# Kernel optimization log

Measured on AMD Instinct MI355X. Metric: run time of the kernel, lower is better.

## Reference

```python
import jax, jax.numpy as jnp
import numpy as np

B, N, E, T, DIN, H, G, ND, NT, L = 4, 10000, 320000, 16, 16, 64, 64, 16, 3, 7


def _mlp2(x, W1, b1, W2, b2):
    # Linear -> LeakyReLU -> (Dropout: eval identity) -> Linear -> LeakyReLU
    h = jax.nn.leaky_relu(x @ W1 + b1)
    return jax.nn.leaky_relu(h @ W2 + b2)


def _gcn_conv(x, src, dst, ew, nt, W1, b1, W2, b2):
    # x: [B,N,D], nt: [B,N,ND], ew: [*,E,1] broadcastable over batch
    x_in = _mlp2(jnp.concatenate([x, nt], axis=-1), W1, b1, W2, b2)  # [B,N,G]
    msgs = x_in[:, src, :] * ew                                      # gather + weight, [B,E,G]
    aggr = jnp.zeros(x_in.shape, x_in.dtype).at[:, dst, :].add(msgs) # scatter-add, [B,N,G]
    return x + aggr


def _gru(x, Wx, Wh, bx, bh):
    # PyTorch-style GRU over time axis. x: [B,N,T,DIN] -> hs: [T,B,N,H]
    xw = jnp.einsum('bntd,dh->tbnh', x, Wx) + bx  # precompute input projections [T,B,N,3H]
    h0 = jnp.zeros(x.shape[:2] + (Wh.shape[0],), x.dtype)

    def step(h, xw_t):
        hw = h @ Wh + bh
        xr, xz, xn = jnp.split(xw_t, 3, axis=-1)
        hr, hz, hn = jnp.split(hw, 3, axis=-1)
        r = jax.nn.sigmoid(xr + hr)
        z = jax.nn.sigmoid(xz + hz)
        n = jnp.tanh(xn + r * hn)
        h_new = (1 - z) * n + z * h
        return h_new, h_new

    _, hs = jax.lax.scan(step, h0, xw)
    return hs


def reference(input_day, edge_attr, gru_Wx, gru_Wh, gru_bx, gru_bh,
              rnn_fc_W, rnn_fc_b,
              e_emb, e_c0_W1, e_c0_b1, e_c0_W2, e_c0_b2,
              e_c1_W1, e_c1_b1, e_c1_W2, e_c1_b2,
              e_fm_W1, e_fm_b1, e_fm_W2, e_fm_b2,
              g_emb, g_c0_W1, g_c0_b1, g_c0_W2, g_c0_b2,
              g_c1_W1, g_c1_b1, g_c1_W2, g_c1_b2,
              gcn_fc_W, gcn_fc_b,
              edge_index, node_type_ids):
    src, dst = edge_index[0], edge_index[1]

    # KRNN encoder (GRU) + max over time + FC head
    hs = _gru(input_day, gru_Wx, gru_Wh, gru_bx, gru_bh)  # [T,B,N,H]
    rnn_out = hs.max(axis=0)                              # kr_out.max(dim=-2) -> [B,N,H]
    y_rnn = rnn_out @ rnn_fc_W + rnn_fc_b                 # [B,N,L]

    # EdgeNet: GCN stack on static edge_attr, then per-edge pair MLP -> gate
    nt_e = jnp.broadcast_to(e_emb[node_type_ids][None], (B, N, ND))
    ew0 = edge_attr.reshape(1, E, 1)
    x = rnn_out
    x = _gcn_conv(x, src, dst, ew0, nt_e, e_c0_W1, e_c0_b1, e_c0_W2, e_c0_b2)
    x = _gcn_conv(x, src, dst, ew0, nt_e, e_c1_W1, e_c1_b1, e_c1_W2, e_c1_b2)
    edge_x = jnp.concatenate([x[:, src, :], x[:, dst, :]], axis=-1)  # [B,E,2G]
    h = jax.nn.leaky_relu(edge_x @ e_fm_W1 + e_fm_b1)
    edge_gate = jax.nn.relu(h @ e_fm_W2 + e_fm_b2)                   # [B,E,1]

    # Main GCNNet with learned edge gates
    nt_g = jnp.broadcast_to(g_emb[node_type_ids][None], (B, N, ND))
    x = rnn_out
    x = _gcn_conv(x, src, dst, edge_gate, nt_g, g_c0_W1, g_c0_b1, g_c0_W2, g_c0_b2)
    x = _gcn_conv(x, src, dst, edge_gate, nt_g, g_c1_W1, g_c1_b1, g_c1_W2, g_c1_b2)
    y_gcn = x @ gcn_fc_W + gcn_fc_b                                  # [B,N,L]

    return y_rnn + y_gcn


def setup_inputs() -> dict:
    key = jax.random.key(0)
    ks = iter(jax.random.split(key, 48))

    def nrm(shape, s=0.1):
        return jax.random.normal(next(ks), shape, jnp.float32) * s

    inp = {}
    inp['input_day'] = jax.random.normal(next(ks), (B, N, T, DIN), jnp.float32)
    inp['edge_index'] = jax.random.randint(next(ks), (2, E), 0, N)
    inp['node_type_ids'] = jax.random.randint(next(ks), (N,), 0, NT)
    inp['edge_attr'] = jax.random.uniform(next(ks), (E,), jnp.float32)

    inp['gru_Wx'] = nrm((DIN, 3 * H))
    inp['gru_Wh'] = nrm((H, 3 * H))
    inp['gru_bx'] = jnp.zeros((3 * H,), jnp.float32)
    inp['gru_bh'] = jnp.zeros((3 * H,), jnp.float32)
    inp['rnn_fc_W'] = nrm((H, L))
    inp['rnn_fc_b'] = jnp.zeros((L,), jnp.float32)

    inp['e_emb'] = nrm((NT, ND))
    inp['g_emb'] = nrm((NT, ND))
    for pre, in_dim in (('e_c0', H + ND), ('e_c1', G + ND), ('g_c0', H + ND), ('g_c1', G + ND)):
        inp[pre + '_W1'] = nrm((in_dim, G))
        inp[pre + '_b1'] = jnp.zeros((G,), jnp.float32)
        inp[pre + '_W2'] = nrm((G, G))
        inp[pre + '_b2'] = jnp.zeros((G,), jnp.float32)

    inp['e_fm_W1'] = nrm((2 * G, G))
    inp['e_fm_b1'] = jnp.zeros((G,), jnp.float32)
    inp['e_fm_W2'] = nrm((G, 1))
    inp['e_fm_b2'] = jnp.zeros((1,), jnp.float32)

    inp['gcn_fc_W'] = nrm((G, L))
    inp['gcn_fc_b'] = jnp.zeros((L,), jnp.float32)
    return inp
```

## Files before the change

kernel.cpp:

```cpp
#include <hip/hip_runtime.h>
#include <hip/hip_bf16.h>

#define NB 4
#define NN 10000
#define NE 320000
#define BN 40000
#define NL 7

typedef float f32x4 __attribute__((ext_vector_type(4)));
typedef __bf16 bf16x8 __attribute__((ext_vector_type(8)));

__device__ __forceinline__ float bf2f(unsigned short u){
  unsigned x = ((unsigned)u) << 16;
  return __builtin_bit_cast(float, x);
}
__device__ __forceinline__ unsigned short f2bf(float f){
  unsigned u = __builtin_bit_cast(unsigned, f);
  u += 0x7fffu + ((u >> 16) & 1u);
  return (unsigned short)(u >> 16);
}
__device__ __forceinline__ bf16x8 zero8(){
  uint4 z = make_uint4(0u,0u,0u,0u);
  return __builtin_bit_cast(bf16x8, z);
}
__device__ __forceinline__ bf16x8 one8(){
  uint4 z = make_uint4(0x3f80u,0u,0u,0u);
  return __builtin_bit_cast(bf16x8, z);
}
__device__ __forceinline__ bf16x8 ld8bf(const unsigned short* p){
  uint4 u = *(const uint4*)p;
  return __builtin_bit_cast(bf16x8, u);
}
__device__ __forceinline__ unsigned pk2(float lo, float hi){
  unsigned r;
  asm("v_cvt_pk_bf16_f32 %0, %1, %2" : "=v"(r) : "v"(lo), "v"(hi));
  return r;
}
__device__ __forceinline__ bf16x8 ld8f(const float* p){
  float4 a = *(const float4*)p;
  float4 b = *(const float4*)(p+4);
  uint4 u = make_uint4(pk2(a.x,a.y), pk2(a.z,a.w), pk2(b.x,b.y), pk2(b.z,b.w));
  return __builtin_bit_cast(bf16x8, u);
}
__device__ __forceinline__ float frcp(float x){ return __builtin_amdgcn_rcpf(x); }
__device__ __forceinline__ float tanh_(float x){ return 1.f - 2.f*frcp(__expf(2.f*x)+1.f); }
__device__ __forceinline__ float lrelu(float x){ return x > 0.f ? x : 0.01f*x; }

#define LDS_WAIT() asm volatile("s_waitcnt lgkmcnt(0)" ::: "memory")

#define WT_SET   10240
#define WT_UV    40960
#define WT_TOTAL 49152

__device__ __forceinline__ void mlp2_body(
    int bid,
    const float* __restrict__ x,
    const int* __restrict__ ntid,
    const float* __restrict__ emb,
    const unsigned short* __restrict__ W1T,
    const float* __restrict__ b1,
    const unsigned short* __restrict__ W2T,
    const float* __restrict__ b2,
    unsigned short* __restrict__ out)
{
  __shared__ __attribute__((aligned(16))) unsigned short hb[4][16][72];
  int tid = threadIdx.x;
  int wave = tid>>6, lane = tid&63, ln16 = lane&15, quad = lane>>4;
  int row0 = bid*64 + wave*16;
  int r_ = row0 + ln16;
  const float* xr = x + (size_t)r_*64;
  bf16x8 a0 = ld8f(xr + quad*8);
  bf16x8 a1 = ld8f(xr + 32 + quad*8);
  int id = ntid[r_ % NN];
  bf16x8 a2 = (quad<2) ? ld8f(emb + id*16 + quad*8) : zero8();

  f32x4 acc[4];
  #pragma unroll
  for (int nt=0;nt<4;++nt){
    float bb = b1[nt*16+ln16];
    acc[nt] = (f32x4){bb,bb,bb,bb};
    acc[nt] = __builtin_amdgcn_mfma_f32_16x16x32_bf16(a0, ld8bf(W1T + (nt*16+ln16)*96 + quad*8),      acc[nt], 0,0,0);
    acc[nt] = __builtin_amdgcn_mfma_f32_16x16x32_bf16(a1, ld8bf(W1T + (nt*16+ln16)*96 + 32 + quad*8), acc[nt], 0,0,0);
    acc[nt] = __builtin_amdgcn_mfma_f32_16x16x32_bf16(a2, ld8bf(W1T + (nt*16+ln16)*96 + 64 + quad*8), acc[nt], 0,0,0);
  }
  #pragma unroll
  for (int nt=0;nt<4;++nt)
    #pragma unroll
    for (int i=0;i<4;++i)
      hb[wave][quad*4+i][nt*16+ln16] = f2bf(lrelu(acc[nt][i]));
  LDS_WAIT();
  bf16x8 h0 = ld8bf(&hb[wave][ln16][quad*8]);
  bf16x8 h1 = ld8bf(&hb[wave][ln16][32+quad*8]);
  f32x4 acc2[4];
  #pragma unroll
  for (int nt=0;nt<4;++nt){
    float bb = b2[nt*16+ln16];
    acc2[nt] = (f32x4){bb,bb,bb,bb};
    acc2[nt] = __builtin_amdgcn_mfma_f32_16x16x32_bf16(h0, ld8bf(W2T + (nt*16+ln16)*64 + quad*8),      acc2[nt], 0,0,0);
    acc2[nt] = __builtin_amdgcn_mfma_f32_16x16x32_bf16(h1, ld8bf(W2T + (nt*16+ln16)*64 + 32 + quad*8), acc2[nt], 0,0,0);
  }
  #pragma unroll
  for (int nt=0;nt<4;++nt)
    #pragma unroll
    for (int i=0;i<4;++i)
      out[(size_t)(row0+quad*4+i)*64 + nt*16+ln16] = f2bf(lrelu(acc2[nt][i]));
}

__global__ __launch_bounds__(256, 2) void gru_count_kernel(
    const float* __restrict__ xd,
    const float* __restrict__ Wx,
    const float* __restrict__ Wh,
    const float* __restrict__ bx,
    const float* __restrict__ bh,
    float* __restrict__ rnn,
    const int* __restrict__ ei,
    int* __restrict__ counts,
    const float* __restrict__ ec0W1, const float* __restrict__ ec0W2,
    const float* __restrict__ ec1W1, const float* __restrict__ ec1W2,
    const float* __restrict__ gc0W1, const float* __restrict__ gc0W2,
    const float* __restrict__ gc1W1, const float* __restrict__ gc1W2,
    const float* __restrict__ efmW1,
    unsigned short* __restrict__ wt)
{
  if (blockIdx.x >= 1875){
    int pidx = blockIdx.x - 1875;
    for (int i = pidx*256 + threadIdx.x; i < WT_TOTAL; i += 2048){
      unsigned short v;
      if (i < WT_UV){
        int s = i / WT_SET, j = i - s*WT_SET;
        const float* W1s = (s==0) ? ec0W1 : (s==1) ? ec1W1 : (s==2) ? gc0W1 : gc1W1;
        const float* W2s = (s==0) ? ec0W2 : (s==1) ? ec1W2 : (s==2) ? gc0W2 : gc1W2;
        if (j < 6144){
          int n = j / 96, k = j - n*96;
          v = (k < 80) ? f2bf(W1s[k*64+n]) : (unsigned short)0;
        } else {
          int j2 = j - 6144;
          int n = j2 >> 6, k = j2 & 63;
          v = f2bf(W2s[k*64+n]);
        }
      } else {
        int j = i - WT_UV;
        int n = j >> 6, k = j & 63;
        v = f2bf((n < 64) ? efmW1[k*64+n] : efmW1[4096 + k*64 + (n-64)]);
      }
      wt[i] = v;
    }
    return;
  }
  if (blockIdx.x >= 625){
    int e = (blockIdx.x-625)*256 + threadIdx.x;
    atomicAdd(&counts[ei[NE+e]], 1);
    return;
  }
  __shared__ __attribute__((aligned(16))) unsigned short WhT[192][72];
  __shared__ __attribute__((aligned(16))) unsigned short WxT[192][40];
  __shared__ __attribute__((aligned(16))) unsigned short hb[4][16][76];
  int tid = threadIdx.x;
  int wave = tid >> 6, lane = tid & 63;
  int ln16 = lane & 15, quad = lane >> 4;

  for (int i = tid; i < 64*192; i += 256){
    int k = i / 192, n = i - k*192;
    WhT[n][k] = f2bf(Wh[i]);
  }
  for (int i = tid; i < 16*192; i += 256){
    int k = i / 192, n = i - k*192;
    WxT[n][k] = f2bf(Wx[i]);
    WxT[n][17+k] = 0;
  }
  if (tid < 192){
    float bias = (tid < 128) ? (bx[tid] + bh[tid]) : bx[tid];
    WxT[tid][16] = f2bf(bias);
  }
  for (int i = tid; i < 4*16*76; i += 256) ((unsigned short*)hb)[i] = 0;
  __syncthreads();

  int rowbase = blockIdx.x * 64 + wave * 16;

  bf16x8 whf[2][12];
  #pragma unroll
  for (int kt=0; kt<2; ++kt)
    #pragma unroll
    for (int nt=0; nt<12; ++nt)
      whf[kt][nt] = ld8bf(&WhT[nt*16 + ln16][kt*32 + quad*8]);

  f32x4 bhn2[4];
  #pragma unroll
  for (int j=0;j<4;++j)
    bhn2[j] = *(const f32x4*)(bh + 128 + j*16 + quad*4);

  f32x4 hprev[4], vmax[4];
  #pragma unroll
  for (int j=0;j<4;++j){
    hprev[j] = (f32x4){0.f,0.f,0.f,0.f};
    vmax[j]  = (f32x4){-1e30f,-1e30f,-1e30f,-1e30f};
  }

  const float* xrow = xd + (size_t)(rowbase + ln16) * 256;
  unsigned short* hrow = &hb[wave][ln16][0];

  bf16x8 axc;
  if (quad < 2) axc = ld8f(xrow + quad*8);
  else          axc = (quad == 2) ? one8() : zero8();

  for (int t = 0; t < 16; ++t){
    bf16x8 axn;
    if (quad < 2) axn = (t < 15) ? ld8f(xrow + (t+1)*16 + quad*8) : zero8();
    else          axn = (quad == 2) ? one8() : zero8();
    bf16x8 ah0 = ld8bf(hrow + quad*8);
    bf16x8 ah1 = ld8bf(hrow + 32 + quad*8);

    #pragma unroll
    for (int j=0;j<4;++j){
      bf16x8 xr = ld8bf(&WxT[j*16+ln16][quad*8]);
      bf16x8 xz = ld8bf(&WxT[(4+j)*16+ln16][quad*8]);
      bf16x8 xn = ld8bf(&WxT[(8+j)*16+ln16][quad*8]);
      f32x4 z4 = (f32x4){0.f,0.f,0.f,0.f};
      f32x4 ar = __builtin_amdgcn_mfma_f32_16x16x32_bf16(xr, axc, z4, 0,0,0);
      ar = __builtin_amdgcn_mfma_f32_16x16x32_bf16(whf[0][j], ah0, ar, 0,0,0);
      ar = __builtin_amdgcn_mfma_f32_16x16x32_bf16(whf[1][j], ah1, ar, 0,0,0);
      f32x4 az = __builtin_amdgcn_mfma_f32_16x16x32_bf16(xz, axc, z4, 0,0,0);
      az = __builtin_amdgcn_mfma_f32_16x16x32_bf16(whf[0][4+j], ah0, az, 0,0,0);
      az = __builtin_amdgcn_mfma_f32_16x16x32_bf16(whf[1][4+j], ah1, az, 0,0,0);
      f32x4 an = __builtin_amdgcn_mfma_f32_16x16x32_bf16(xn, axc, z4, 0,0,0);
      f32x4 ah = __builtin_amdgcn_mfma_f32_16x16x32_bf16(whf[0][8+j], ah0, bhn2[j], 0,0,0);
      ah = __builtin_amdgcn_mfma_f32_16x16x32_bf16(whf[1][8+j], ah1, ah, 0,0,0);
      f32x4 hv;
      #pragma unroll
      for (int i=0;i<4;++i){
        float Er = __expf(-ar[i]);
        float Ez = __expf(-az[i]);
        float pr = 1.f + Er, pz = 1.f + Ez;
        float D  = frcp(pr * pz);
        float r  = D * pz;
        float z  = D * pr;
        float nn = tanh_(an[i] + r * ah[i]);
        float h  = fmaf(z, hprev[j][i]-nn, nn);
        hprev[j][i] = h;
        vmax[j][i] = fmaxf(vmax[j][i], h);
        hv[i] = h;
      }
      *(uint2*)&hb[wave][ln16][j*16+quad*4] = make_uint2(pk2(hv[0],hv[1]), pk2(hv[2],hv[3]));
    }
    LDS_WAIT();
    axc = axn;
  }
  float* orow = rnn + (size_t)(rowbase + ln16)*64;
  #pragma unroll
  for (int j=0;j<4;++j)
    *(f32x4*)(orow + j*16 + quad*4) = vmax[j];
}

__global__ __launch_bounds__(1024) void scan_kernel(const int* __restrict__ counts,
                                                    int* __restrict__ rowptr, int* __restrict__ cursor){
  __shared__ int incl[10240];
  __shared__ int wsum[16];
  int tid=threadIdx.x, wave=tid>>6, lane=tid&63;
  int base = wave*640;
  int carry=0;
  #pragma unroll
  for (int c=0;c<10;++c){
    int i = base + c*64 + lane;
    int v = (i<NN)? counts[i] : 0;
    int s = v;
    #pragma unroll
    for (int off=1;off<64;off<<=1){
      int t_ = __shfl_up(s, off);
      if (lane>=off) s += t_;
    }
    s += carry;
    incl[base + c*64 + lane] = s;
    carry = __shfl(s, 63);
  }
  if (lane==63) wsum[wave]=carry;
  __syncthreads();
  if (wave==0){
    int w_ = (lane<16)? wsum[lane]:0;
    #pragma unroll
    for (int off=1;off<16;off<<=1){
      int t_ = __shfl_up(w_, off);
      if (lane>=off) w_ += t_;
    }
    if (lane<16) wsum[lane]=w_;
  }
  __syncthreads();
  int woff = (wave>0)? wsum[wave-1] : 0;
  #pragma unroll
  for (int c=0;c<10;++c){
    int i = base + c*64 + lane;
    if (i<NN){
      int excl = incl[i] + woff - counts[i];
      rowptr[i]=excl; cursor[i]=excl;
    }
  }
  if (tid==0) rowptr[NN]=wsum[15];
}

__global__ __launch_bounds__(256) void fill_mlp2e_kernel(
    const int* __restrict__ ei,
    const float* __restrict__ ea,
    int* __restrict__ cursor,
    int* __restrict__ ssrc,
    float* __restrict__ wcsr,
    const float* __restrict__ x,
    const int* __restrict__ ntid,
    const float* __restrict__ emb,
    const unsigned short* __restrict__ wt,
    const float* __restrict__ b1, const float* __restrict__ b2,
    unsigned short* __restrict__ out)
{
  if (blockIdx.x >= 625){
    int e = (blockIdx.x-625)*256 + threadIdx.x;
    int d = ei[NE+e];
    int pos = atomicAdd(&cursor[d],1);
    ssrc[pos]=ei[e];
    wcsr[pos]=ea[e];
    return;
  }
  mlp2_body(blockIdx.x, x, ntid, emb, wt, b1, wt + 6144, b2, out);
}

__global__ __launch_bounds__(256) void aggr_mlp_kernel(
    const float* __restrict__ x,
    const unsigned short* __restrict__ xin,
    const int* __restrict__ rowptr,
    const int* __restrict__ ssrc,
    const float* __restrict__ wp,
    int bstride,
    const int* __restrict__ ntid,
    const float* __restrict__ emb,
    const unsigned short* __restrict__ W1T,
    const float* __restrict__ b1,
    const unsigned short* __restrict__ W2T,
    const float* __restrict__ b2,
    float* __restrict__ xe_out,
    unsigned short* __restrict__ out)
{
  int u = blockIdx.x;
  int b = (u & 7) >> 1;
  int m = ((u >> 3) << 1) | (u & 1);
  if (m >= 625) return;
  int row0 = b*NN + m*16;

  __shared__ __attribute__((aligned(16))) unsigned short hb[16][72];
  __shared__ __attribute__((aligned(16))) unsigned short h2[16][72];
  int tid = threadIdx.x;
  int wave = tid>>6, lane = tid&63, ln16 = lane&15, quad = lane>>4;
  int r = wave*4 + quad;
  int row = row0 + r;
  int n = m*16 + r;
  int l = ln16;
  int p0 = rowptr[n], p1 = rowptr[n+1];
  const unsigned short* xb_ = xin + (size_t)b*NN*64;
  const float* wb = wp + (size_t)b*bstride;
  float a0=0.f, a1=0.f, a2=0.f, a3=0.f;
  #pragma unroll 4
  for (int p=p0; p<p1; ++p){
    int s = ssrc[p];
    float w = wb[p];
    uint2 mm = *(const uint2*)(xb_ + (size_t)s*64 + l*4);
    a0 += bf2f((unsigned short)(mm.x & 0xffffu)) * w;
    a1 += bf2f((unsigned short)(mm.x >> 16)) * w;
    a2 += bf2f((unsigned short)(mm.y & 0xffffu)) * w;
    a3 += bf2f((unsigned short)(mm.y >> 16)) * w;
  }
  float4 base = *(const float4*)(x + (size_t)row*64 + l*4);
  float o0=base.x+a0, o1=base.y+a1, o2=base.z+a2, o3=base.w+a3;
  float4 ov; ov.x=o0; ov.y=o1; ov.z=o2; ov.w=o3;
  *(float4*)(xe_out + (size_t)row*64 + l*4) = ov;
  *(uint2*)&hb[r][l*4] = make_uint2(pk2(o0,o1), pk2(o2,o3));
  __syncthreads();

  int id = ntid[m*16 + ln16];
  bf16x8 xa0 = ld8bf(&hb[ln16][quad*8]);
  bf16x8 xa1 = ld8bf(&hb[ln16][32+quad*8]);
  bf16x8 xa2 = (quad<2) ? ld8f(emb + id*16 + quad*8) : zero8();
  float bb = b1[wave*16+ln16];
  f32x4 acc = (f32x4){bb,bb,bb,bb};
  acc = __builtin_amdgcn_mfma_f32_16x16x32_bf16(xa0, ld8bf(W1T + (wave*16+ln16)*96 + quad*8),      acc, 0,0,0);
  acc = __builtin_amdgcn_mfma_f32_16x16x32_bf16(xa1, ld8bf(W1T + (wave*16+ln16)*96 + 32 + quad*8), acc, 0,0,0);
  acc = __builtin_amdgcn_mfma_f32_16x16x32_bf16(xa2, ld8bf(W1T + (wave*16+ln16)*96 + 64 + quad*8), acc, 0,0,0);
  #pragma unroll
  for (int i=0;i<4;++i)
    h2[quad*4+i][wave*16+ln16] = f2bf(lrelu(acc[i]));
  __syncthreads();
  bf16x8 hh0 = ld8bf(&h2[ln16][quad*8]);
  bf16x8 hh1 = ld8bf(&h2[ln16][32+quad*8]);
  float b2v = b2[wave*16+ln16];
  f32x4 acc2 = (f32x4){b2v,b2v,b2v,b2v};
  acc2 = __builtin_amdgcn_mfma_f32_16x16x32_bf16(hh0, ld8bf(W2T + (wave*16+ln16)*64 + quad*8),      acc2, 0,0,0);
  acc2 = __builtin_amdgcn_mfma_f32_16x16x32_bf16(hh1, ld8bf(W2T + (wave*16+ln16)*64 + 32 + quad*8), acc2, 0,0,0);
  #pragma unroll
  for (int i=0;i<4;++i)
    out[(size_t)(row0+quad*4+i)*64 + wave*16+ln16] = f2bf(lrelu(acc2[i]));
}

__global__ __launch_bounds__(256) void aggr_uv_kernel(
    const float* __restrict__ x,
    const unsigned short* __restrict__ xin,
    const int* __restrict__ rowptr,
    const int* __restrict__ ssrc,
    const float* __restrict__ wp,
    int bstride,
    const unsigned short* __restrict__ WT,
    unsigned short* __restrict__ uvp)
{
  int u = blockIdx.x;
  int b = (u & 7) >> 1;
  int m = ((u >> 3) << 1) | (u & 1);
  if (m >= 625) return;
  int row0 = b*NN + m*16;

  __shared__ __attribute__((aligned(16))) unsigned short hb[16][72];
  int tid = threadIdx.x;
  int wave = tid>>6, lane = tid&63, ln16 = lane&15, quad = lane>>4;
  int r = wave*4 + quad;
  int row = row0 + r;
  int n = m*16 + r;
  int l = ln16;
  int p0 = rowptr[n], p1 = rowptr[n+1];
  const unsigned short* xb_ = xin + (size_t)b*NN*64;
  const float* wb = wp + (size_t)b*bstride;
  float a0=0.f, a1=0.f, a2=0.f, a3=0.f;
  #pragma unroll 4
  for (int p=p0; p<p1; ++p){
    int s = ssrc[p];
    float w = wb[p];
    uint2 mm = *(const uint2*)(xb_ + (size_t)s*64 + l*4);
    a0 += bf2f((unsigned short)(mm.x & 0xffffu)) * w;
    a1 += bf2f((unsigned short)(mm.x >> 16)) * w;
    a2 += bf2f((unsigned short)(mm.y & 0xffffu)) * w;
    a3 += bf2f((unsigned short)(mm.y >> 16)) * w;
  }
  float4 base = *(const float4*)(x + (size_t)row*64 + l*4);
  float o0=base.x+a0, o1=base.y+a1, o2=base.z+a2, o3=base.w+a3;
  *(uint2*)&hb[r][l*4] = make_uint2(pk2(o0,o1), pk2(o2,o3));
  __syncthreads();

  bf16x8 xa0 = ld8bf(&hb[ln16][quad*8]);
  bf16x8 xa1 = ld8bf(&hb[ln16][32+quad*8]);
  #pragma unroll
  for (int t=0;t<2;++t){
    int nt = wave*2 + t;
    f32x4 acc = (f32x4){0.f,0.f,0.f,0.f};
    acc = __builtin_amdgcn_mfma_f32_16x16x32_bf16(xa0, ld8bf(WT + (nt*16+ln16)*64 + quad*8),      acc, 0,0,0);
    acc = __builtin_amdgcn_mfma_f32_16x16x32_bf16(xa1, ld8bf(WT + (nt*16+ln16)*64 + 32 + quad*8), acc, 0,0,0);
    #pragma unroll
    for (int i=0;i<4;++i)
      uvp[(size_t)(row0+quad*4+i)*128 + nt*16+ln16] = f2bf(acc[i]);
  }
}

__global__ __launch_bounds__(256) void gate_mlp2g_kernel(
    const unsigned short* __restrict__ uvp,
    const int* __restrict__ rowptr,
    const int* __restrict__ ssrc,
    const float* __restrict__ b1,
    const float* __restrict__ W2g,
    const float* __restrict__ b2,
    float* __restrict__ gate,
    const float* __restrict__ x,
    const int* __restrict__ ntid,
    const float* __restrict__ emb,
    const unsigned short* __restrict__ wtg,
    const float* __restrict__ mb1, const float* __restrict__ mb2,
    unsigned short* __restrict__ mout)
{
  if (blockIdx.x < 625){
    mlp2_body(blockIdx.x, x, ntid, emb, wtg, mb1, wtg + 6144, mb2, mout);
    return;
  }
  int u = blockIdx.x;
  int b = (u & 7) >> 1;
  int m = (((u - 625) >> 3) << 1) | (u & 1);
  if (m >= 2500) return;
  int tid=threadIdx.x;
  int wave=tid>>6, lane=tid&63;
  int sub=lane>>4, l=lane&15;
  int n = m*4 + wave;
  int p0 = rowptr[n], p1 = rowptr[n+1];
  const unsigned short* ub = uvp + (size_t)b*NN*128;
  uint2 vu = *(const uint2*)(ub + (size_t)n*128 + 64 + l*4);
  float v0=bf2f((unsigned short)(vu.x&0xffffu)), v1=bf2f((unsigned short)(vu.x>>16));
  float v2=bf2f((unsigned short)(vu.y&0xffffu)), v3=bf2f((unsigned short)(vu.y>>16));
  float4 bb = *(const float4*)(b1 + l*4);
  float4 ww = *(const float4*)(W2g + l*4);
  float b2v = b2[0];
  float* gb = gate + (size_t)b*NE;
  #pragma unroll 4
  for (int p=p0+sub; p<p1; p+=4){
    int s = ssrc[p];
    uint2 uu = *(const uint2*)(ub + (size_t)s*128 + l*4);
    float h0 = lrelu(bf2f((unsigned short)(uu.x&0xffffu)) + v0 + bb.x);
    float h1 = lrelu(bf2f((unsigned short)(uu.x>>16))     + v1 + bb.y);
    float h2 = lrelu(bf2f((unsigned short)(uu.y&0xffffu)) + v2 + bb.z);
    float h3 = lrelu(bf2f((unsigned short)(uu.y>>16))     + v3 + bb.w);
    float part = h0*ww.x + h1*ww.y + h2*ww.z + h3*ww.w;
    part += __shfl_xor(part,1);
    part += __shfl_xor(part,2);
    part += __shfl_xor(part,4);
    part += __shfl_xor(part,8);
    if (l==0){
      float g = part + b2v;
      gb[p] = g>0.f ? g : 0.f;
    }
  }
}

__global__ __launch_bounds__(256) void aggr_final_kernel(
    const float* x,
    const unsigned short* __restrict__ xin,
    const int* __restrict__ rowptr,
    const int* __restrict__ ssrc,
    const float* __restrict__ wp,
    const float* __restrict__ rnn,
    const float* __restrict__ Wr, const float* __restrict__ br,
    const float* __restrict__ Wg, const float* __restrict__ bg,
    float* __restrict__ out)
{
  int u = blockIdx.x;
  int b = (u & 7) >> 1;
  int m = ((u >> 3) << 1) | (u & 1);
  if (m >= 2500) return;

  __shared__ float sWr[448], sWg[448], sb[7];
  int tid=threadIdx.x;
  for (int i=tid;i<448;i+=256){ sWr[i]=Wr[i]; sWg[i]=Wg[i]; }
  if (tid<7) sb[tid]=br[tid]+bg[tid];
  __syncthreads();
  int wave=tid>>6, lane=tid&63;
  int sub=lane>>4, l=lane&15;
  int n = m*4 + wave;
  int bid = b*NN + n;
  int p0 = rowptr[n], p1 = rowptr[n+1];
  const unsigned short* xb_ = xin + (size_t)b*NN*64;
  const float* wb = wp + (size_t)b*NE;
  float a0=0.f, a1=0.f, a2=0.f, a3=0.f;
  #pragma unroll 4
  for (int p=p0+sub; p<p1; p+=4){
    int s = ssrc[p];
    float w = wb[p];
    uint2 mm = *(const uint2*)(xb_ + (size_t)s*64 + l*4);
    a0 += bf2f((unsigned short)(mm.x & 0xffffu)) * w;
    a1 += bf2f((unsigned short)(mm.x >> 16)) * w;
    a2 += bf2f((unsigned short)(mm.y & 0xffffu)) * w;
    a3 += bf2f((unsigned short)(mm.y >> 16)) * w;
  }
  a0 += __shfl_xor(a0,16); a0 += __shfl_xor(a0,32);
  a1 += __shfl_xor(a1,16); a1 += __shfl_xor(a1,32);
  a2 += __shfl_xor(a2,16); a2 += __shfl_xor(a2,32);
  a3 += __shfl_xor(a3,16); a3 += __shfl_xor(a3,32);
  if (sub==0){
    float4 base = *(const float4*)(x + (size_t)bid*64 + l*4);
    float o0=base.x+a0, o1=base.y+a1, o2=base.z+a2, o3=base.w+a3;
    float4 rr = *(const float4*)(rnn + (size_t)bid*64 + l*4);
    float part[7];
    #pragma unroll
    for (int q=0;q<7;++q)
      part[q] = o0*sWg[(l*4+0)*7+q] + o1*sWg[(l*4+1)*7+q]
              + o2*sWg[(l*4+2)*7+q] + o3*sWg[(l*4+3)*7+q]
              + rr.x*sWr[(l*4+0)*7+q] + rr.y*sWr[(l*4+1)*7+q]
              + rr.z*sWr[(l*4+2)*7+q] + rr.w*sWr[(l*4+3)*7+q];
    #pragma unroll
    for (int q=0;q<7;++q){
      part[q] += __shfl_xor(part[q],1);
      part[q] += __shfl_xor(part[q],2);
      part[q] += __shfl_xor(part[q],4);
      part[q] += __shfl_xor(part[q],8);
    }
    if (l==0){
      #pragma unroll
      for (int q=0;q<7;++q) out[(size_t)bid*7+q] = part[q] + sb[q];
    }
  }
}

extern "C" void kernel_launch(void* const* d_in, const int* in_sizes, int n_in,
                              void* d_out, int out_size, void* d_ws, size_t ws_size,
                              hipStream_t stream)
{
  (void)in_sizes; (void)n_in; (void)out_size; (void)ws_size;
  const float* input_day = (const float*)d_in[0];
  const int* ei    = (const int*)d_in[1];
  const int* ntid  = (const int*)d_in[2];
  const float* edge_attr = (const float*)d_in[3];
  const float* gWx = (const float*)d_in[4];
  const float* gWh = (const float*)d_in[5];
  const float* gbx = (const float*)d_in[6];
  const float* gbh = (const float*)d_in[7];
  const float* rW  = (const float*)d_in[8];
  const float* rb  = (const float*)d_in[9];
  const float* eemb= (const float*)d_in[10];
  const float* gemb= (const float*)d_in[11];
  const float* ec0W1=(const float*)d_in[12];
  const float* ec0b1=(const float*)d_in[13];
  const float* ec0W2=(const float*)d_in[14];
  const float* ec0b2=(const float*)d_in[15];
  const float* ec1W1=(const float*)d_in[16];
  const float* ec1b1=(const float*)d_in[17];
  const float* ec1W2=(const float*)d_in[18];
  const float* ec1b2=(const float*)d_in[19];
  const float* gc0W1=(const float*)d_in[20];
  const float* gc0b1=(const float*)d_in[21];
  const float* gc0W2=(const float*)d_in[22];
  const float* gc0b2=(const float*)d_in[23];
  const float* gc1W1=(const float*)d_in[24];
  const float* gc1b1=(const float*)d_in[25];
  const float* gc1W2=(const float*)d_in[26];
  const float* gc1b2=(const float*)d_in[27];
  const float* efmW1=(const float*)d_in[28];
  const float* efmb1=(const float*)d_in[29];
  const float* efmW2=(const float*)d_in[30];
  const float* efmb2=(const float*)d_in[31];
  const float* gcnW =(const float*)d_in[32];
  const float* gcnb =(const float*)d_in[33];

  char* ws = (char*)d_ws;
  float*          rnn = (float*)(ws);
  float*          xe  = (float*)(ws + 10240000);
  unsigned short* xinA= (unsigned short*)(ws + 20480000);
  unsigned short* uvp = (unsigned short*)(ws + 25600000);
  float*          gat = (float*)(ws + 35840000);
  int* rowptr= (int*)(ws + 40960000);
  int* cursor= (int*)(ws + 41000064);
  int* counts= (int*)(ws + 41040064);
  int*   ssrc= (int*)(ws + 41080064);
  float* wcsr= (float*)(ws + 42360064);
  unsigned short* xinB = (unsigned short*)gat;
  unsigned short* xinD = (unsigned short*)uvp;
  unsigned short* wt   = (unsigned short*)d_out;

  hipMemsetAsync(counts, 0, NN*sizeof(int), stream);
  gru_count_kernel<<<1883, 256, 0, stream>>>(input_day, gWx, gWh, gbx, gbh, rnn,
                                             ei, counts,
                                             ec0W1, ec0W2, ec1W1, ec1W2,
                                             gc0W1, gc0W2, gc1W1, gc1W2,
                                             efmW1, wt);
  scan_kernel<<<1, 1024, 0, stream>>>(counts, rowptr, cursor);
  fill_mlp2e_kernel<<<1875, 256, 0, stream>>>(ei, edge_attr, cursor, ssrc, wcsr,
                                              rnn, ntid, eemb,
                                              wt, ec0b1, ec0b2, xinA);
  aggr_mlp_kernel<<<2504, 256, 0, stream>>>(rnn, xinA, rowptr, ssrc, wcsr, 0,
                                            ntid, eemb,
                                            wt + WT_SET, ec1b1, wt + WT_SET + 6144, ec1b2,
                                            xe, xinB);
  aggr_uv_kernel<<<2504, 256, 0, stream>>>(xe, xinB, rowptr, ssrc, wcsr, 0,
                                           wt + WT_UV, uvp);
  gate_mlp2g_kernel<<<10633, 256, 0, stream>>>(uvp, rowptr, ssrc,
                                               efmb1, efmW2, efmb2, gat,
                                               rnn, ntid, gemb,
                                               wt + 2*WT_SET, gc0b1, gc0b2, xinA);
  aggr_mlp_kernel<<<2504, 256, 0, stream>>>(rnn, xinA, rowptr, ssrc, gat, NE,
                                            ntid, gemb,
                                            wt + 3*WT_SET, gc1b1, wt + 3*WT_SET + 6144, gc1b2,
                                            xe, xinD);
  aggr_final_kernel<<<10008, 256, 0, stream>>>(xe, xinD, rowptr, ssrc, gat, rnn,
                                               rW, rb, gcnW, gcnb, (float*)d_out);
}
```

Before: 419.2 us.

## Fuse edge gate computation into GCN aggregation kernels, dropping gate buffer

The separate gate kernel, which wrote a per-edge gate array, is removed. Each of the two consumer aggregation kernels now recomputes the gate inline from the uv projections while gathering neighbour features. The g_c0 MLP blocks are moved into the uv kernel launch. This removes a launch and the gate array write and reads, but the gate is computed twice, and each aggregation loop now does an extra gather of uvp rows plus shuffle reductions per edge.

```diff
diff --git a/kernel.cpp b/kernel.cpp
--- a/kernel.cpp
+++ b/kernel.cpp
@@ -395,7 +395,101 @@
     out[(size_t)(row0+quad*4+i)*64 + wave*16+ln16] = f2bf(lrelu(acc2[i]));
 }
 
-__global__ __launch_bounds__(256) void aggr_uv_kernel(
+__global__ __launch_bounds__(256) void aggr_mlp_gate_kernel(
+    const float* __restrict__ x,
+    const unsigned short* __restrict__ xin,
+    const int* __restrict__ rowptr,
+    const int* __restrict__ ssrc,
+    const unsigned short* __restrict__ uvp,
+    const float* __restrict__ gb1,
+    const float* __restrict__ gW2,
+    const float* __restrict__ gb2,
+    const int* __restrict__ ntid,
+    const float* __restrict__ emb,
+    const unsigned short* __restrict__ W1T,
+    const float* __restrict__ b1,
+    const unsigned short* __restrict__ W2T,
+    const float* __restrict__ b2,
+    float* __restrict__ xe_out,
+    unsigned short* __restrict__ out)
+{
+  int u = blockIdx.x;
+  int b = (u & 7) >> 1;
+  int m = ((u >> 3) << 1) | (u & 1);
+  if (m >= 625) return;
+  int row0 = b*NN + m*16;
+
+  __shared__ __attribute__((aligned(16))) unsigned short hb[16][72];
+  __shared__ __attribute__((aligned(16))) unsigned short h2[16][72];
+  int tid = threadIdx.x;
+  int wave = tid>>6, lane = tid&63, ln16 = lane&15, quad = lane>>4;
+  int r = wave*4 + quad;
+  int row = row0 + r;
+  int n = m*16 + r;
+  int l = ln16;
+  int p0 = rowptr[n], p1 = rowptr[n+1];
+  const unsigned short* xb_ = xin + (size_t)b*NN*64;
+  const unsigned short* ub  = uvp + (size_t)b*NN*128;
+  uint2 vv = *(const uint2*)(ub + (size_t)n*128 + 64 + l*4);
+  float v0=bf2f((unsigned short)(vv.x&0xffffu)), v1=bf2f((unsigned short)(vv.x>>16));
+  float v2=bf2f((unsigned short)(vv.y&0xffffu)), v3=bf2f((unsigned short)(vv.y>>16));
+  float4 bb4 = *(const float4*)(gb1 + l*4);
+  float4 ww4 = *(const float4*)(gW2 + l*4);
+  float gb2v = gb2[0];
+  float a0=0.f, a1=0.f, a2=0.f, a3=0.f;
+  #pragma unroll 4
+  for (int p=p0; p<p1; ++p){
+    int s = ssrc[p];
+    uint2 mm = *(const uint2*)(xb_ + (size_t)s*64 + l*4);
+    uint2 uu = *(const uint2*)(ub  + (size_t)s*128 + l*4);
+    float h0 = lrelu(bf2f((unsigned short)(uu.x&0xffffu)) + v0 + bb4.x);
+    float h1 = lrelu(bf2f((unsigned short)(uu.x>>16))     + v1 + bb4.y);
+    float h2_ = lrelu(bf2f((unsigned short)(uu.y&0xffffu)) + v2 + bb4.z);
+    float h3 = lrelu(bf2f((unsigned short)(uu.y>>16))     + v3 + bb4.w);
+    float part = h0*ww4.x + h1*ww4.y + h2_*ww4.z + h3*ww4.w;
+    part += __shfl_xor(part,1);
+    part += __shfl_xor(part,2);
+    part += __shfl_xor(part,4);
+    part += __shfl_xor(part,8);
+    float g = part + gb2v;
+    g = g>0.f ? g : 0.f;
+    a0 += bf2f((unsigned short)(mm.x & 0xffffu)) * g;
+    a1 += bf2f((unsigned short)(mm.x >> 16)) * g;
+    a2 += bf2f((unsigned short)(mm.y & 0xffffu)) * g;
+    a3 += bf2f((unsigned short)(mm.y >> 16)) * g;
+  }
+  float4 base = *(const float4*)(x + (size_t)row*64 + l*4);
+  float o0=base.x+a0, o1=base.y+a1, o2=base.z+a2, o3=base.w+a3;
+  float4 ov; ov.x=o0; ov.y=o1; ov.z=o2; ov.w=o3;
+  *(float4*)(xe_out + (size_t)row*64 + l*4) = ov;
+  *(uint2*)&hb[r][l*4] = make_uint2(pk2(o0,o1), pk2(o2,o3));
+  __syncthreads();
+
+  int id = ntid[m*16 + ln16];
+  bf16x8 xa0 = ld8bf(&hb[ln16][quad*8]);
+  bf16x8 xa1 = ld8bf(&hb[ln16][32+quad*8]);
+  bf16x8 xa2 = (quad<2) ? ld8f(emb + id*16 + quad*8) : zero8();
+  float bb = b1[wave*16+ln16];
+  f32x4 acc = (f32x4){bb,bb,bb,bb};
+  acc = __builtin_amdgcn_mfma_f32_16x16x32_bf16(xa0, ld8bf(W1T + (wave*16+ln16)*96 + quad*8),      acc, 0,0,0);
+  acc = __builtin_amdgcn_mfma_f32_16x16x32_bf16(xa1, ld8bf(W1T + (wave*16+ln16)*96 + 32 + quad*8), acc, 0,0,0);
+  acc = __builtin_amdgcn_mfma_f32_16x16x32_bf16(xa2, ld8bf(W1T + (wave*16+ln16)*96 + 64 + quad*8), acc, 0,0,0);
+  #pragma unroll
+  for (int i=0;i<4;++i)
+    h2[quad*4+i][wave*16+ln16] = f2bf(lrelu(acc[i]));
+  __syncthreads();
+  bf16x8 hh0 = ld8bf(&h2[ln16][quad*8]);
+  bf16x8 hh1 = ld8bf(&h2[ln16][32+quad*8]);
+  float b2v = b2[wave*16+ln16];
+  f32x4 acc2 = (f32x4){b2v,b2v,b2v,b2v};
+  acc2 = __builtin_amdgcn_mfma_f32_16x16x32_bf16(hh0, ld8bf(W2T + (wave*16+ln16)*64 + quad*8),      acc2, 0,0,0);
+  acc2 = __builtin_amdgcn_mfma_f32_16x16x32_bf16(hh1, ld8bf(W2T + (wave*16+ln16)*64 + 32 + quad*8), acc2, 0,0,0);
+  #pragma unroll
+  for (int i=0;i<4;++i)
+    out[(size_t)(row0+quad*4+i)*64 + wave*16+ln16] = f2bf(lrelu(acc2[i]));
+}
+
+__global__ __launch_bounds__(256) void aggr_uv_mlp2g_kernel(
     const float* __restrict__ x,
     const unsigned short* __restrict__ xin,
     const int* __restrict__ rowptr,
@@ -403,15 +497,25 @@
     const float* __restrict__ wp,
     int bstride,
     const unsigned short* __restrict__ WT,
-    unsigned short* __restrict__ uvp)
+    unsigned short* __restrict__ uvp,
+    const float* __restrict__ rnn,
+    const int* __restrict__ ntid,
+    const float* __restrict__ gemb,
+    const unsigned short* __restrict__ wtg,
+    const float* __restrict__ gc0b1, const float* __restrict__ gc0b2,
+    unsigned short* __restrict__ xinA)
 {
   int u = blockIdx.x;
+  if (u >= 2504){
+    mlp2_body(u - 2504, rnn, ntid, gemb, wtg, gc0b1, wtg + 6144, gc0b2, xinA);
+    return;
+  }
   int b = (u & 7) >> 1;
   int m = ((u >> 3) << 1) | (u & 1);
   if (m >= 625) return;
   int row0 = b*NN + m*16;
 
-  __shared__ __attribute__((aligned(16))) unsigned short hb[16][72];
+  __shared__ __attribute__((aligned(16))) unsigned short hbu[16][72];
   int tid = threadIdx.x;
   int wave = tid>>6, lane = tid&63, ln16 = lane&15, quad = lane>>4;
   int r = wave*4 + quad;
@@ -434,11 +538,11 @@
   }
   float4 base = *(const float4*)(x + (size_t)row*64 + l*4);
   float o0=base.x+a0, o1=base.y+a1, o2=base.z+a2, o3=base.w+a3;
-  *(uint2*)&hb[r][l*4] = make_uint2(pk2(o0,o1), pk2(o2,o3));
-  __syncthreads();
-
-  bf16x8 xa0 = ld8bf(&hb[ln16][quad*8]);
-  bf16x8 xa1 = ld8bf(&hb[ln16][32+quad*8]);
+  *(uint2*)&hbu[r][l*4] = make_uint2(pk2(o0,o1), pk2(o2,o3));
+  __syncthreads();
+
+  bf16x8 xa0 = ld8bf(&hbu[ln16][quad*8]);
+  bf16x8 xa1 = ld8bf(&hbu[ln16][32+quad*8]);
   #pragma unroll
   for (int t=0;t<2;++t){
     int nt = wave*2 + t;
@@ -451,68 +555,15 @@
   }
 }
 
-__global__ __launch_bounds__(256) void gate_mlp2g_kernel(
-    const unsigned short* __restrict__ uvp,
-    const int* __restrict__ rowptr,
-    const int* __restrict__ ssrc,
-    const float* __restrict__ b1,
-    const float* __restrict__ W2g,
-    const float* __restrict__ b2,
-    float* __restrict__ gate,
-    const float* __restrict__ x,
-    const int* __restrict__ ntid,
-    const float* __restrict__ emb,
-    const unsigned short* __restrict__ wtg,
-    const float* __restrict__ mb1, const float* __restrict__ mb2,
-    unsigned short* __restrict__ mout)
-{
-  if (blockIdx.x < 625){
-    mlp2_body(blockIdx.x, x, ntid, emb, wtg, mb1, wtg + 6144, mb2, mout);
-    return;
-  }
-  int u = blockIdx.x;
-  int b = (u & 7) >> 1;
-  int m = (((u - 625) >> 3) << 1) | (u & 1);
-  if (m >= 2500) return;
-  int tid=threadIdx.x;
-  int wave=tid>>6, lane=tid&63;
-  int sub=lane>>4, l=lane&15;
-  int n = m*4 + wave;
-  int p0 = rowptr[n], p1 = rowptr[n+1];
-  const unsigned short* ub = uvp + (size_t)b*NN*128;
-  uint2 vu = *(const uint2*)(ub + (size_t)n*128 + 64 + l*4);
-  float v0=bf2f((unsigned short)(vu.x&0xffffu)), v1=bf2f((unsigned short)(vu.x>>16));
-  float v2=bf2f((unsigned short)(vu.y&0xffffu)), v3=bf2f((unsigned short)(vu.y>>16));
-  float4 bb = *(const float4*)(b1 + l*4);
-  float4 ww = *(const float4*)(W2g + l*4);
-  float b2v = b2[0];
-  float* gb = gate + (size_t)b*NE;
-  #pragma unroll 4
-  for (int p=p0+sub; p<p1; p+=4){
-    int s = ssrc[p];
-    uint2 uu = *(const uint2*)(ub + (size_t)s*128 + l*4);
-    float h0 = lrelu(bf2f((unsigned short)(uu.x&0xffffu)) + v0 + bb.x);
-    float h1 = lrelu(bf2f((unsigned short)(uu.x>>16))     + v1 + bb.y);
-    float h2 = lrelu(bf2f((unsigned short)(uu.y&0xffffu)) + v2 + bb.z);
-    float h3 = lrelu(bf2f((unsigned short)(uu.y>>16))     + v3 + bb.w);
-    float part = h0*ww.x + h1*ww.y + h2*ww.z + h3*ww.w;
-    part += __shfl_xor(part,1);
-    part += __shfl_xor(part,2);
-    part += __shfl_xor(part,4);
-    part += __shfl_xor(part,8);
-    if (l==0){
-      float g = part + b2v;
-      gb[p] = g>0.f ? g : 0.f;
-    }
-  }
-}
-
 __global__ __launch_bounds__(256) void aggr_final_kernel(
     const float* x,
     const unsigned short* __restrict__ xin,
     const int* __restrict__ rowptr,
     const int* __restrict__ ssrc,
-    const float* __restrict__ wp,
+    const unsigned short* __restrict__ uvp,
+    const float* __restrict__ gb1,
+    const float* __restrict__ gW2,
+    const float* __restrict__ gb2,
     const float* __restrict__ rnn,
     const float* __restrict__ Wr, const float* __restrict__ br,
     const float* __restrict__ Wg, const float* __restrict__ bg,
@@ -534,17 +585,34 @@
   int bid = b*NN + n;
   int p0 = rowptr[n], p1 = rowptr[n+1];
   const unsigned short* xb_ = xin + (size_t)b*NN*64;
-  const float* wb = wp + (size_t)b*NE;
+  const unsigned short* ub  = uvp + (size_t)b*NN*128;
+  uint2 vv = *(const uint2*)(ub + (size_t)n*128 + 64 + l*4);
+  float v0=bf2f((unsigned short)(vv.x&0xffffu)), v1=bf2f((unsigned short)(vv.x>>16));
+  float v2=bf2f((unsigned short)(vv.y&0xffffu)), v3=bf2f((unsigned short)(vv.y>>16));
+  float4 bb4 = *(const float4*)(gb1 + l*4);
+  float4 ww4 = *(const float4*)(gW2 + l*4);
+  float gb2v = gb2[0];
   float a0=0.f, a1=0.f, a2=0.f, a3=0.f;
   #pragma unroll 4
   for (int p=p0+sub; p<p1; p+=4){
     int s = ssrc[p];
-    float w = wb[p];
     uint2 mm = *(const uint2*)(xb_ + (size_t)s*64 + l*4);
-    a0 += bf2f((unsigned short)(mm.x & 0xffffu)) * w;
-    a1 += bf2f((unsigned short)(mm.x >> 16)) * w;
-    a2 += bf2f((unsigned short)(mm.y & 0xffffu)) * w;
-    a3 += bf2f((unsigned short)(mm.y >> 16)) * w;
+    uint2 uu = *(const uint2*)(ub  + (size_t)s*128 + l*4);
+    float h0 = lrelu(bf2f((unsigned short)(uu.x&0xffffu)) + v0 + bb4.x);
+    float h1 = lrelu(bf2f((unsigned short)(uu.x>>16))     + v1 + bb4.y);
+    float h2 = lrelu(bf2f((unsigned short)(uu.y&0xffffu)) + v2 + bb4.z);
+    float h3 = lrelu(bf2f((unsigned short)(uu.y>>16))     + v3 + bb4.w);
+    float part = h0*ww4.x + h1*ww4.y + h2*ww4.z + h3*ww4.w;
+    part += __shfl_xor(part,1);
+    part += __shfl_xor(part,2);
+    part += __shfl_xor(part,4);
+    part += __shfl_xor(part,8);
+    float g = part + gb2v;
+    g = g>0.f ? g : 0.f;
+    a0 += bf2f((unsigned short)(mm.x & 0xffffu)) * g;
+    a1 += bf2f((unsigned short)(mm.x >> 16)) * g;
+    a2 += bf2f((unsigned short)(mm.y & 0xffffu)) * g;
+    a3 += bf2f((unsigned short)(mm.y >> 16)) * g;
   }
   a0 += __shfl_xor(a0,16); a0 += __shfl_xor(a0,32);
   a1 += __shfl_xor(a1,16); a1 += __shfl_xor(a1,32);
@@ -627,7 +695,7 @@
   int*   ssrc= (int*)(ws + 41080064);
   float* wcsr= (float*)(ws + 42360064);
   unsigned short* xinB = (unsigned short*)gat;
-  unsigned short* xinD = (unsigned short*)uvp;
+  unsigned short* xinD = (unsigned short*)gat;
   unsigned short* wt   = (unsigned short*)d_out;
 
   hipMemsetAsync(counts, 0, NN*sizeof(int), stream);
@@ -644,16 +712,16 @@
                                             ntid, eemb,
                                             wt + WT_SET, ec1b1, wt + WT_SET + 6144, ec1b2,
                                             xe, xinB);
-  aggr_uv_kernel<<<2504, 256, 0, stream>>>(xe, xinB, rowptr, ssrc, wcsr, 0,
-                                           wt + WT_UV, uvp);
-  gate_mlp2g_kernel<<<10633, 256, 0, stream>>>(uvp, rowptr, ssrc,
-                                               efmb1, efmW2, efmb2, gat,
-                                               rnn, ntid, gemb,
-                                               wt + 2*WT_SET, gc0b1, gc0b2, xinA);
-  aggr_mlp_kernel<<<2504, 256, 0, stream>>>(rnn, xinA, rowptr, ssrc, gat, NE,
-                                            ntid, gemb,
-                                            wt + 3*WT_SET, gc1b1, wt + 3*WT_SET + 6144, gc1b2,
-                                            xe, xinD);
-  aggr_final_kernel<<<10008, 256, 0, stream>>>(xe, xinD, rowptr, ssrc, gat, rnn,
+  aggr_uv_mlp2g_kernel<<<3129, 256, 0, stream>>>(xe, xinB, rowptr, ssrc, wcsr, 0,
+                                                 wt + WT_UV, uvp,
+                                                 rnn, ntid, gemb,
+                                                 wt + 2*WT_SET, gc0b1, gc0b2, xinA);
+  aggr_mlp_gate_kernel<<<2504, 256, 0, stream>>>(rnn, xinA, rowptr, ssrc,
+                                                 uvp, efmb1, efmW2, efmb2,
+                                                 ntid, gemb,
+                                                 wt + 3*WT_SET, gc1b1, wt + 3*WT_SET + 6144, gc1b2,
+                                                 xe, xinD);
+  aggr_final_kernel<<<10008, 256, 0, stream>>>(xe, xinD, rowptr, ssrc,
+                                               uvp, efmb1, efmW2, efmb2, rnn,
                                                rW, rb, gcnW, gcnb, (float*)d_out);
 }
```

After: 430.8 us. 2.8% more time.
